# Optimization experiments

Measured on AMD Instinct MI355X. Metric: run time of the kernel, lower is better.

Reference implementation:

```python
import jax, jax.numpy as jnp
import numpy as np

FRAME_T = 8
NUM_K = 10


def _masked_att(att, temp):
    # att: [B, H, P, P] -> softmax over groups of size P//FRAME_T, top-k threshold mask
    B, H, P, _ = att.shape
    D = P // FRAME_T
    a = att.reshape(B, H, P, FRAME_T, D)
    a = jax.nn.softmax(a / temp, axis=-1)
    # k-th largest value per row as threshold (torch.topk values are sorted desc)
    margin = jax.lax.top_k(a, NUM_K)[0][..., -1]  # [B,H,P,FRAME_T]
    a = a * (a >= margin[..., None])
    return a  # [B,H,P,FRAME_T,D]


def setup_inputs() -> dict:
    key = jax.random.key(0)
    k1, k2, k3, k4 = jax.random.split(key, 4)
    B, H, P, hd = 4, 12, 1568, 64
    return {
        "att_s": jax.random.normal(k1, (B, H, P, P), dtype=jnp.float32),
        "att_t": jax.random.normal(k2, (B, H, P, P), dtype=jnp.float32),
        "v_s": jax.random.normal(k3, (B, H, P, hd), dtype=jnp.float32),
        "v_t": jax.random.normal(k4, (B, H, P, hd), dtype=jnp.float32),
    }


def reference(att_s, att_t, v_s, v_t):
    temp = jnp.float32(1.0)
    B, H, P, _ = att_t.shape
    H_s = att_s.shape[1]
    h_dim = v_t.shape[-1]
    D = P // FRAME_T

    a_s = _masked_att(att_s, temp)  # [B,Hs,P,T,D]
    a_t = _masked_att(att_t, temp)  # [B,H,P,T,D]

    vt = v_t.reshape(B, H, D, FRAME_T, h_dim)
    vs = v_s.reshape(B, H_s, D, FRAME_T, h_dim)

    norm_s = a_s.sum(-1)  # [B,Hs,P,T]
    norm_t = a_t.sum(-1)

    o_s = jnp.einsum('bhptd,bhdte->bhpte', a_s, vs) / norm_s[..., None]
    o_t = jnp.einsum('bhptd,bhdte->bhpte', a_t, vt) / norm_t[..., None]

    loss = jnp.mean((o_s - o_t) ** 2)
    return loss
```

## Files before the change

kernel.cpp:

```cpp
#include <hip/hip_runtime.h>
#include <hip/hip_bf16.h>

#define PP 1568
#define TT 8
#define DD 196
#define HD 64
#define NBH 48
#define NROW (NBH*PP*TT)
#define RPB 32
#define NBLK3 (NROW/RPB)
#define NRED1 ((NBLK3+255)/256)
#define SUB (8*DD*4)
#define VSLAB (DD*TT*HD)
#define BPB 392
#define KMASK 0xFFFFFF00u

typedef float f4 __attribute__((ext_vector_type(4)));
typedef unsigned u4 __attribute__((ext_vector_type(4)));

__device__ __forceinline__ float readlane_f(float v, int l) {
    return __int_as_float(__builtin_amdgcn_readlane(__float_as_int(v), l));
}

__device__ __forceinline__ float wave_sum_u(float v) {
#define STEPS(ctrl) { float t_ = __int_as_float(__builtin_amdgcn_update_dpp( \
        0, __float_as_int(v), ctrl, 0xF, 0xF, true)); v += t_; }
    STEPS(0x111) STEPS(0x112) STEPS(0x114) STEPS(0x118) STEPS(0x142) STEPS(0x143)
#undef STEPS
    return readlane_f(v, 63);
}

__device__ __forceinline__ unsigned UMX(unsigned a, unsigned b){ return a>b?a:b; }
__device__ __forceinline__ unsigned UMN(unsigned a, unsigned b){ return a<b?a:b; }

__device__ __forceinline__ float untr(unsigned u) {
    return (u & 0x80000000u) ? __uint_as_float(u ^ 0x80000000u)
                             : __uint_as_float(~u);
}

struct K6  { unsigned k0,k1,k2,k3,k4,k5; };
struct K10 { unsigned k0,k1,k2,k3,k4,k5,k6,k7,k8,k9; };
struct MR  { K10 f; unsigned mx; };

#define INSK(Y,C) { unsigned mx_=UMX((Y),(C)), mn_=UMN((Y),(C)); (Y)=mx_; (C)=mn_; }
#define PUTK6(Q,X,D) { unsigned b_=__float_as_uint(X); \
  unsigned u_=b_^((unsigned)((int)b_>>31)|0x80000000u); \
  unsigned c_=(u_&KMASK)|(unsigned)(D); \
  INSK(Q.k0,c_) INSK(Q.k1,c_) INSK(Q.k2,c_) INSK(Q.k3,c_) INSK(Q.k4,c_) INSK(Q.k5,c_) }
#define PUT4K6(Q,V,D0) PUTK6(Q,(V).x,(D0)) PUTK6(Q,(V).y,(D0)+1) \
                       PUTK6(Q,(V).z,(D0)+2) PUTK6(Q,(V).w,(D0)+3)

__device__ __forceinline__ K6 chain_rows(const char* stg, int a, int b8) {
    K6 q = {0,0,0,0,0,0};
    const char* rb = stg + a*784 + b8*16;
    f4 v;
    v = *(const f4*)(rb);       PUT4K6(q, v, b8*4)
    v = *(const f4*)(rb+128);   PUT4K6(q, v, b8*4+32)
    v = *(const f4*)(rb+256);   PUT4K6(q, v, b8*4+64)
    v = *(const f4*)(rb+384);   PUT4K6(q, v, b8*4+96)
    v = *(const f4*)(rb+512);   PUT4K6(q, v, b8*4+128)
    v = *(const f4*)(rb+640);   PUT4K6(q, v, b8*4+160)
    if (b8 == 7) { v = *(const f4*)(stg + a*784 + 768); PUT4K6(q, v, 192) }
    return q;
}

#define SWZ(x, pat) (unsigned)__builtin_amdgcn_ds_swizzle((int)(x), pat)
__device__ __forceinline__ K6 kshuf8_6(K6 a) {
    K6 r;
    r.k0=SWZ(a.k0,0x201F); r.k1=SWZ(a.k1,0x201F); r.k2=SWZ(a.k2,0x201F);
    r.k3=SWZ(a.k3,0x201F); r.k4=SWZ(a.k4,0x201F); r.k5=SWZ(a.k5,0x201F);
    return r;
}
__device__ __forceinline__ K10 kshuf16(K10 a) {
    K10 r;
    r.k0=SWZ(a.k0,0x401F); r.k1=SWZ(a.k1,0x401F); r.k2=SWZ(a.k2,0x401F);
    r.k3=SWZ(a.k3,0x401F); r.k4=SWZ(a.k4,0x401F); r.k5=SWZ(a.k5,0x401F);
    r.k6=SWZ(a.k6,0x401F); r.k7=SWZ(a.k7,0x401F); r.k8=SWZ(a.k8,0x401F);
    r.k9=SWZ(a.k9,0x401F);
    return r;
}
__device__ __forceinline__ K10 kbp32(K10 a, int bpx) {
    K10 r;
    r.k0=(unsigned)__builtin_amdgcn_ds_bpermute(bpx,(int)a.k0);
    r.k1=(unsigned)__builtin_amdgcn_ds_bpermute(bpx,(int)a.k1);
    r.k2=(unsigned)__builtin_amdgcn_ds_bpermute(bpx,(int)a.k2);
    r.k3=(unsigned)__builtin_amdgcn_ds_bpermute(bpx,(int)a.k3);
    r.k4=(unsigned)__builtin_amdgcn_ds_bpermute(bpx,(int)a.k4);
    r.k5=(unsigned)__builtin_amdgcn_ds_bpermute(bpx,(int)a.k5);
    r.k6=(unsigned)__builtin_amdgcn_ds_bpermute(bpx,(int)a.k6);
    r.k7=(unsigned)__builtin_amdgcn_ds_bpermute(bpx,(int)a.k7);
    r.k8=(unsigned)__builtin_amdgcn_ds_bpermute(bpx,(int)a.k8);
    r.k9=(unsigned)__builtin_amdgcn_ds_bpermute(bpx,(int)a.k9);
    return r;
}

__device__ __forceinline__ K10 kmrg66(K6 A, K6 B) {
    unsigned p00=UMN(A.k0,B.k0);
    unsigned p01=UMN(A.k0,B.k1), p10=UMN(A.k1,B.k0);
    unsigned p02=UMN(A.k0,B.k2), p11=UMN(A.k1,B.k1), p20=UMN(A.k2,B.k0);
    unsigned p03=UMN(A.k0,B.k3), p12=UMN(A.k1,B.k2), p21=UMN(A.k2,B.k1), p30=UMN(A.k3,B.k0);
    unsigned p04=UMN(A.k0,B.k4), p13=UMN(A.k1,B.k3), p22=UMN(A.k2,B.k2), p31=UMN(A.k3,B.k1), p40=UMN(A.k4,B.k0);
    unsigned p05=UMN(A.k0,B.k5), p14=UMN(A.k1,B.k4), p23=UMN(A.k2,B.k3), p32=UMN(A.k3,B.k2), p41=UMN(A.k4,B.k1), p50=UMN(A.k5,B.k0);
    unsigned p15=UMN(A.k1,B.k5), p24=UMN(A.k2,B.k4), p33=UMN(A.k3,B.k3), p42=UMN(A.k4,B.k2), p51=UMN(A.k5,B.k1);
    unsigned p25=UMN(A.k2,B.k5), p34=UMN(A.k3,B.k4), p43=UMN(A.k4,B.k3), p52=UMN(A.k5,B.k2);
    unsigned p35=UMN(A.k3,B.k5), p44=UMN(A.k4,B.k4), p53=UMN(A.k5,B.k3);
    K10 M;
    M.k0=UMX(A.k0,B.k0);
    M.k1=UMX(UMX(A.k1,B.k1),p00);
    M.k2=UMX(UMX(A.k2,B.k2),UMX(p01,p10));
    M.k3=UMX(UMX(A.k3,B.k3),UMX(p02,UMX(p11,p20)));
    M.k4=UMX(UMX(A.k4,B.k4),UMX(UMX(p03,p12),UMX(p21,p30)));
    M.k5=UMX(UMX(A.k5,B.k5),UMX(UMX(p04,p13),UMX(p22,UMX(p31,p40))));
    M.k6=UMX(UMX(p05,p14),UMX(UMX(p23,p32),UMX(p41,p50)));
    M.k7=UMX(UMX(p15,p24),UMX(p33,UMX(p42,p51)));
    M.k8=UMX(UMX(p25,p34),UMX(p43,p52));
    M.k9=UMX(p35,UMX(p44,p53));
    return M;
}

__device__ __forceinline__ K10 kmrg(K10 A, K10 B) {
    unsigned p00=UMN(A.k0,B.k0);
    unsigned p01=UMN(A.k0,B.k1), p10=UMN(A.k1,B.k0);
    unsigned p02=UMN(A.k0,B.k2), p11=UMN(A.k1,B.k1), p20=UMN(A.k2,B.k0);
    unsigned p03=UMN(A.k0,B.k3), p12=UMN(A.k1,B.k2), p21=UMN(A.k2,B.k1), p30=UMN(A.k3,B.k0);
    unsigned p04=UMN(A.k0,B.k4), p13=UMN(A.k1,B.k3), p22=UMN(A.k2,B.k2), p31=UMN(A.k3,B.k1), p40=UMN(A.k4,B.k0);
    unsigned p05=UMN(A.k0,B.k5), p14=UMN(A.k1,B.k4), p23=UMN(A.k2,B.k3), p32=UMN(A.k3,B.k2), p41=UMN(A.k4,B.k1), p50=UMN(A.k5,B.k0);
    unsigned p06=UMN(A.k0,B.k6), p15=UMN(A.k1,B.k5), p24=UMN(A.k2,B.k4), p33=UMN(A.k3,B.k3), p42=UMN(A.k4,B.k2), p51=UMN(A.k5,B.k1), p60=UMN(A.k6,B.k0);
    unsigned p07=UMN(A.k0,B.k7), p16=UMN(A.k1,B.k6), p25=UMN(A.k2,B.k5), p34=UMN(A.k3,B.k4), p43=UMN(A.k4,B.k3), p52=UMN(A.k5,B.k2), p61=UMN(A.k6,B.k1), p70=UMN(A.k7,B.k0);
    unsigned p08=UMN(A.k0,B.k8), p17=UMN(A.k1,B.k7), p26=UMN(A.k2,B.k6), p35=UMN(A.k3,B.k5), p44=UMN(A.k4,B.k4), p53=UMN(A.k5,B.k3), p62=UMN(A.k6,B.k2), p71=UMN(A.k7,B.k1), p80=UMN(A.k8,B.k0);
    K10 M;
    M.k0=UMX(A.k0,B.k0);
    M.k1=UMX(UMX(A.k1,B.k1),p00);
    M.k2=UMX(UMX(A.k2,B.k2),UMX(p01,p10));
    M.k3=UMX(UMX(A.k3,B.k3),UMX(p02,UMX(p11,p20)));
    M.k4=UMX(UMX(A.k4,B.k4),UMX(UMX(p03,p12),UMX(p21,p30)));
    M.k5=UMX(UMX(A.k5,B.k5),UMX(UMX(p04,p13),UMX(p22,UMX(p31,p40))));
    M.k6=UMX(UMX(A.k6,B.k6),UMX(UMX(p05,p14),UMX(UMX(p23,p32),UMX(p41,p50))));
    M.k7=UMX(UMX(A.k7,B.k7),UMX(UMX(UMX(p06,p15),UMX(p24,p33)),UMX(UMX(p42,p51),p60)));
    M.k8=UMX(UMX(A.k8,B.k8),UMX(UMX(UMX(p07,p16),UMX(p25,p34)),UMX(UMX(p43,p52),UMX(p61,p70))));
    M.k9=UMX(UMX(A.k9,B.k9),UMX(UMX(UMX(p08,p17),UMX(p26,p35)),UMX(UMX(p44,p53),UMX(UMX(p62,p71),p80))));
    return M;
}

__device__ __forceinline__ MR merge_all(K6 q, int bpx) {
    K10 m = kmrg66(q, kshuf8_6(q));
    K10 n = kmrg(m, kshuf16(m));
    K10 r = kbp32(n, bpx);
    MR out;
    out.mx = UMX(n.k0, r.k0);
    out.f.k0=UMX(n.k0,r.k9); out.f.k1=UMX(n.k1,r.k8); out.f.k2=UMX(n.k2,r.k7);
    out.f.k3=UMX(n.k3,r.k6); out.f.k4=UMX(n.k4,r.k5); out.f.k5=UMX(n.k5,r.k4);
    out.f.k6=UMX(n.k6,r.k3); out.f.k7=UMX(n.k7,r.k2); out.f.k8=UMX(n.k8,r.k1);
    out.f.k9=UMX(n.k9,r.k0);
    return out;
}

#define LOADR(R, P) { const char* p_=(P); \
    R##0=*(const f4*)(p_+lane*16); \
    R##1=*(const f4*)(p_+1024+lane*16); \
    R##2=*(const f4*)(p_+2048+lane*16); \
    R##3=*(const f4*)(p_+3072+lane*16); \
    R##4=*(const f4*)(p_+4096+lane*16); \
    R##5=*(const f4*)(p_+5120+lane*16); \
    if (lane<8) R##6=*(const f4*)(p_+6144+lane*16); }
#define STORER(R) { \
    *(f4*)(stg+lane*16)=R##0; *(f4*)(stg+1024+lane*16)=R##1; \
    *(f4*)(stg+2048+lane*16)=R##2; *(f4*)(stg+3072+lane*16)=R##3; \
    *(f4*)(stg+4096+lane*16)=R##4; *(f4*)(stg+5120+lane*16)=R##5; \
    if (lane<8) *(f4*)(stg+6144+lane*16)=R##6; }

#define OFS(K) ((((K)&0xFFu)<<9) + t64)

__global__ __launch_bounds__(64, 4) void vtop_main(
        const float* __restrict__ att_s, const float* __restrict__ att_t,
        const float* __restrict__ v_s,   const float* __restrict__ v_t,
        float* __restrict__ partial) {
    __shared__ f4 stgv[SUB/16];
    __shared__ f4 wbuf[5][RPB];
    __shared__ u4 obuf[5][RPB];
    char* stg = (char*)stgv;

    int lane = threadIdx.x;
    int blk  = blockIdx.x;
    int a = lane & 7, b8 = lane >> 3;
    int bpx = (lane ^ 32) << 2;

    const char* baseS = (const char*)att_s + (size_t)blk * (RPB*DD*4);
    const char* baseT = (const char*)att_t + (size_t)blk * (RPB*DD*4);

    f4 rs0{},rs1{},rs2{},rs3{},rs4{},rs5{},rs6{};
    f4 rt0{},rt1{},rt2{},rt3{},rt4{},rt5{},rt6{};

    LOADR(rs, baseS)

#pragma unroll 1
    for (int s = 0; s < 4; ++s) {
        STORER(rs)
        LOADR(rt, baseT + s*SUB)
        K6 qS = chain_rows(stg, a, b8);
        MR mS = merge_all(qS, bpx);
        STORER(rt)
        if (s < 3) LOADR(rs, baseS + (s+1)*SUB)
        K6 qT = chain_rows(stg, a, b8);
        MR mT = merge_all(qT, bpx);
        K10 fS = mS.f, fT = mT.f;

        float CS = untr(mS.mx & KMASK), CT = untr(mT.mx & KMASK);
        float wS0=__expf(untr(fS.k0&KMASK)-CS), wS1=__expf(untr(fS.k1&KMASK)-CS),
              wS2=__expf(untr(fS.k2&KMASK)-CS), wS3=__expf(untr(fS.k3&KMASK)-CS),
              wS4=__expf(untr(fS.k4&KMASK)-CS), wS5=__expf(untr(fS.k5&KMASK)-CS),
              wS6=__expf(untr(fS.k6&KMASK)-CS), wS7=__expf(untr(fS.k7&KMASK)-CS),
              wS8=__expf(untr(fS.k8&KMASK)-CS), wS9=__expf(untr(fS.k9&KMASK)-CS);
        float wT0=__expf(untr(fT.k0&KMASK)-CT), wT1=__expf(untr(fT.k1&KMASK)-CT),
              wT2=__expf(untr(fT.k2&KMASK)-CT), wT3=__expf(untr(fT.k3&KMASK)-CT),
              wT4=__expf(untr(fT.k4&KMASK)-CT), wT5=__expf(untr(fT.k5&KMASK)-CT),
              wT6=__expf(untr(fT.k6&KMASK)-CT), wT7=__expf(untr(fT.k7&KMASK)-CT),
              wT8=__expf(untr(fT.k8&KMASK)-CT), wT9=__expf(untr(fT.k9&KMASK)-CT);
        float wsS = (((wS0+wS1)+(wS2+wS3))+((wS4+wS5)+(wS6+wS7)))+(wS8+wS9);
        float wsT = (((wT0+wT1)+(wT2+wT3))+((wT4+wT5)+(wT6+wT7)))+(wT8+wT9);
        float invS =  __builtin_amdgcn_rcpf(wsS);
        float invT = -__builtin_amdgcn_rcpf(wsT);

        if (lane < 8) {
            int row = (s << 3) | lane;
            unsigned t64 = (unsigned)lane << 6;
            f4 w; u4 o;
            w.x=wS0*invS; w.y=wS1*invS; w.z=wS2*invS; w.w=wS3*invS; wbuf[0][row]=w;
            w.x=wS4*invS; w.y=wS5*invS; w.z=wS6*invS; w.w=wS7*invS; wbuf[1][row]=w;
            w.x=wS8*invS; w.y=wS9*invS; w.z=wT0*invT; w.w=wT1*invT; wbuf[2][row]=w;
            w.x=wT2*invT; w.y=wT3*invT; w.z=wT4*invT; w.w=wT5*invT; wbuf[3][row]=w;
            w.x=wT6*invT; w.y=wT7*invT; w.z=wT8*invT; w.w=wT9*invT; wbuf[4][row]=w;
            o.x=OFS(fS.k0); o.y=OFS(fS.k1); o.z=OFS(fS.k2); o.w=OFS(fS.k3); obuf[0][row]=o;
            o.x=OFS(fS.k4); o.y=OFS(fS.k5); o.z=OFS(fS.k6); o.w=OFS(fS.k7); obuf[1][row]=o;
            o.x=OFS(fS.k8); o.y=OFS(fS.k9); o.z=OFS(fT.k0); o.w=OFS(fT.k1); obuf[2][row]=o;
            o.x=OFS(fT.k2); o.y=OFS(fT.k3); o.z=OFS(fT.k4); o.w=OFS(fT.k5); obuf[3][row]=o;
            o.x=OFS(fT.k6); o.y=OFS(fT.k7); o.z=OFS(fT.k8); o.w=OFS(fT.k9); obuf[4][row]=o;
        }
    }

    int bh = blk / BPB;
    const float* vSb = v_s + (size_t)bh * VSLAB;
    const float* vTb = v_t + (size_t)bh * VSLAB;
    unsigned ul = (unsigned)lane;
    float lacc = 0.f;
#pragma unroll 1
    for (int k = 0; k < RPB; ++k) {
        f4 w0v=wbuf[0][k], w1v=wbuf[1][k], w2v=wbuf[2][k],
           w3v=wbuf[3][k], w4v=wbuf[4][k];
        u4 o0=obuf[0][k], o1=obuf[1][k], o2=obuf[2][k],
           o3=obuf[3][k], o4=obuf[4][k];
        float dsum = 0.f;
#define TERM(WC, OC, VB) dsum = fmaf(WC, VB[(size_t)((OC) + ul)], dsum);
        TERM(w0v.x, o0.x, vSb) TERM(w0v.y, o0.y, vSb)
        TERM(w0v.z, o0.z, vSb) TERM(w0v.w, o0.w, vSb)
        TERM(w1v.x, o1.x, vSb) TERM(w1v.y, o1.y, vSb)
        TERM(w1v.z, o1.z, vSb) TERM(w1v.w, o1.w, vSb)
        TERM(w2v.x, o2.x, vSb) TERM(w2v.y, o2.y, vSb)
        TERM(w2v.z, o2.z, vTb) TERM(w2v.w, o2.w, vTb)
        TERM(w3v.x, o3.x, vTb) TERM(w3v.y, o3.y, vTb)
        TERM(w3v.z, o3.z, vTb) TERM(w3v.w, o3.w, vTb)
        TERM(w4v.x, o4.x, vTb) TERM(w4v.y, o4.y, vTb)
        TERM(w4v.z, o4.z, vTb) TERM(w4v.w, o4.w, vTb)
#undef TERM
        lacc = fmaf(dsum, dsum, lacc);
    }

    float tot = wave_sum_u(lacc);
    if (lane == 0) partial[blk] = tot;
}

__global__ __launch_bounds__(256) void vtop_reduce1(
        const float* __restrict__ partial, float* __restrict__ p2) {
    int i = blockIdx.x * 256 + threadIdx.x;
    float v = (i < NBLK3) ? partial[i] : 0.f;
    float wtot = wave_sum_u(v);
    __shared__ float sm[4];
    int lane = threadIdx.x & 63, wid = threadIdx.x >> 6;
    if (lane == 0) sm[wid] = wtot;
    __syncthreads();
    if (threadIdx.x == 0) p2[blockIdx.x] = (sm[0] + sm[1]) + (sm[2] + sm[3]);
}

__global__ __launch_bounds__(256) void vtop_reduce2(
        const float* __restrict__ p2, float* __restrict__ out) {
    __shared__ double smd[256];
    double a = 0.0;
    if (threadIdx.x < NRED1) a = (double)p2[threadIdx.x];
    smd[threadIdx.x] = a;
    __syncthreads();
    for (int s = 128; s > 0; s >>= 1) {
        if (threadIdx.x < s) smd[threadIdx.x] += smd[threadIdx.x + s];
        __syncthreads();
    }
    if (threadIdx.x == 0) {
        const double inv_n = 1.0 / ((double)NBH * PP * TT * HD);
        out[0] = (float)(smd[0] * inv_n);
    }
}

extern "C" void kernel_launch(void* const* d_in, const int* in_sizes, int n_in,
                              void* d_out, int out_size, void* d_ws, size_t ws_size,
                              hipStream_t stream) {
    const float* att_s = (const float*)d_in[0];
    const float* att_t = (const float*)d_in[1];
    const float* v_s   = (const float*)d_in[2];
    const float* v_t   = (const float*)d_in[3];
    float* out     = (float*)d_out;
    float* partial = (float*)d_ws;
    float* p2      = (float*)d_ws + NBLK3;

    vtop_main<<<NBLK3, 64, 0, stream>>>(att_s, att_t, v_s, v_t, partial);
    vtop_reduce1<<<NRED1, 256, 0, stream>>>(partial, p2);
    vtop_reduce2<<<1, 256, 0, stream>>>(p2, out);
}
```

Before: 352.0 us.

## Read attention rows directly from global memory, pack four waves per block

Drops the LDS staging buffer and the register double-buffering of attention rows. Each lane now reads its strided row segments straight from global memory during the top-k chain. Blocks grow from one wave to four independent waves, each with its own weight/offset LDS slices and its own partial sum, and the reduction sizes are adjusted to match. The aim is to save the LDS round-trip and raise occupancy. In exchange the global loads become less coalesced and the explicit prefetch overlap is lost.

```diff
diff --git a/kernel.cpp b/kernel.cpp
--- a/kernel.cpp
+++ b/kernel.cpp
@@ -7,12 +7,15 @@
 #define HD 64
 #define NBH 48
 #define NROW (NBH*PP*TT)
-#define RPB 32
-#define NBLK3 (NROW/RPB)
-#define NRED1 ((NBLK3+255)/256)
+#define RPW 32
+#define WPB 4
+#define ROWS_PB (RPW*WPB)
+#define NBLK4 (NROW/ROWS_PB)
+#define NPART (NBLK4*WPB)
+#define NRED1 ((NPART+255)/256)
 #define SUB (8*DD*4)
 #define VSLAB (DD*TT*HD)
-#define BPB 392
+#define BPB 98
 #define KMASK 0xFFFFFF00u
 
 typedef float f4 __attribute__((ext_vector_type(4)));
@@ -50,9 +53,9 @@
 #define PUT4K6(Q,V,D0) PUTK6(Q,(V).x,(D0)) PUTK6(Q,(V).y,(D0)+1) \
                        PUTK6(Q,(V).z,(D0)+2) PUTK6(Q,(V).w,(D0)+3)
 
-__device__ __forceinline__ K6 chain_rows(const char* stg, int a, int b8) {
+__device__ __forceinline__ K6 chain_g(const char* base, int a, int b8) {
     K6 q = {0,0,0,0,0,0};
-    const char* rb = stg + a*784 + b8*16;
+    const char* rb = base + a*784 + b8*16;
     f4 v;
     v = *(const f4*)(rb);       PUT4K6(q, v, b8*4)
     v = *(const f4*)(rb+128);   PUT4K6(q, v, b8*4+32)
@@ -60,7 +63,7 @@
     v = *(const f4*)(rb+384);   PUT4K6(q, v, b8*4+96)
     v = *(const f4*)(rb+512);   PUT4K6(q, v, b8*4+128)
     v = *(const f4*)(rb+640);   PUT4K6(q, v, b8*4+160)
-    if (b8 == 7) { v = *(const f4*)(stg + a*784 + 768); PUT4K6(q, v, 192) }
+    if (b8 == 7) { v = *(const f4*)(base + a*784 + 768); PUT4K6(q, v, 192) }
     return q;
 }
 
@@ -155,53 +158,31 @@
     return out;
 }
 
-#define LOADR(R, P) { const char* p_=(P); \
-    R##0=*(const f4*)(p_+lane*16); \
-    R##1=*(const f4*)(p_+1024+lane*16); \
-    R##2=*(const f4*)(p_+2048+lane*16); \
-    R##3=*(const f4*)(p_+3072+lane*16); \
-    R##4=*(const f4*)(p_+4096+lane*16); \
-    R##5=*(const f4*)(p_+5120+lane*16); \
-    if (lane<8) R##6=*(const f4*)(p_+6144+lane*16); }
-#define STORER(R) { \
-    *(f4*)(stg+lane*16)=R##0; *(f4*)(stg+1024+lane*16)=R##1; \
-    *(f4*)(stg+2048+lane*16)=R##2; *(f4*)(stg+3072+lane*16)=R##3; \
-    *(f4*)(stg+4096+lane*16)=R##4; *(f4*)(stg+5120+lane*16)=R##5; \
-    if (lane<8) *(f4*)(stg+6144+lane*16)=R##6; }
-
 #define OFS(K) ((((K)&0xFFu)<<9) + t64)
 
-__global__ __launch_bounds__(64, 4) void vtop_main(
+__global__ __launch_bounds__(256, 7) void vtop_main(
         const float* __restrict__ att_s, const float* __restrict__ att_t,
         const float* __restrict__ v_s,   const float* __restrict__ v_t,
         float* __restrict__ partial) {
-    __shared__ f4 stgv[SUB/16];
-    __shared__ f4 wbuf[5][RPB];
-    __shared__ u4 obuf[5][RPB];
-    char* stg = (char*)stgv;
-
-    int lane = threadIdx.x;
-    int blk  = blockIdx.x;
+    __shared__ f4 wbuf[WPB][5][RPW];
+    __shared__ u4 obuf[WPB][5][RPW];
+
+    int tid  = threadIdx.x;
+    int wid  = tid >> 6;
+    int lane = tid & 63;
     int a = lane & 7, b8 = lane >> 3;
     int bpx = (lane ^ 32) << 2;
-
-    const char* baseS = (const char*)att_s + (size_t)blk * (RPB*DD*4);
-    const char* baseT = (const char*)att_t + (size_t)blk * (RPB*DD*4);
-
-    f4 rs0{},rs1{},rs2{},rs3{},rs4{},rs5{},rs6{};
-    f4 rt0{},rt1{},rt2{},rt3{},rt4{},rt5{},rt6{};
-
-    LOADR(rs, baseS)
+    int blk  = blockIdx.x;
+    int bh   = blk / BPB;
+
+    const char* baseS = (const char*)att_s + ((size_t)blk*ROWS_PB + wid*RPW)*(DD*4);
+    const char* baseT = (const char*)att_t + ((size_t)blk*ROWS_PB + wid*RPW)*(DD*4);
 
 #pragma unroll 1
     for (int s = 0; s < 4; ++s) {
-        STORER(rs)
-        LOADR(rt, baseT + s*SUB)
-        K6 qS = chain_rows(stg, a, b8);
+        K6 qS = chain_g(baseS + s*SUB, a, b8);
         MR mS = merge_all(qS, bpx);
-        STORER(rt)
-        if (s < 3) LOADR(rs, baseS + (s+1)*SUB)
-        K6 qT = chain_rows(stg, a, b8);
+        K6 qT = chain_g(baseT + s*SUB, a, b8);
         MR mT = merge_all(qT, bpx);
         K10 fS = mS.f, fT = mT.f;
 
@@ -225,30 +206,29 @@
             int row = (s << 3) | lane;
             unsigned t64 = (unsigned)lane << 6;
             f4 w; u4 o;
-            w.x=wS0*invS; w.y=wS1*invS; w.z=wS2*invS; w.w=wS3*invS; wbuf[0][row]=w;
-            w.x=wS4*invS; w.y=wS5*invS; w.z=wS6*invS; w.w=wS7*invS; wbuf[1][row]=w;
-            w.x=wS8*invS; w.y=wS9*invS; w.z=wT0*invT; w.w=wT1*invT; wbuf[2][row]=w;
-            w.x=wT2*invT; w.y=wT3*invT; w.z=wT4*invT; w.w=wT5*invT; wbuf[3][row]=w;
-            w.x=wT6*invT; w.y=wT7*invT; w.z=wT8*invT; w.w=wT9*invT; wbuf[4][row]=w;
-            o.x=OFS(fS.k0); o.y=OFS(fS.k1); o.z=OFS(fS.k2); o.w=OFS(fS.k3); obuf[0][row]=o;
-            o.x=OFS(fS.k4); o.y=OFS(fS.k5); o.z=OFS(fS.k6); o.w=OFS(fS.k7); obuf[1][row]=o;
-            o.x=OFS(fS.k8); o.y=OFS(fS.k9); o.z=OFS(fT.k0); o.w=OFS(fT.k1); obuf[2][row]=o;
-            o.x=OFS(fT.k2); o.y=OFS(fT.k3); o.z=OFS(fT.k4); o.w=OFS(fT.k5); obuf[3][row]=o;
-            o.x=OFS(fT.k6); o.y=OFS(fT.k7); o.z=OFS(fT.k8); o.w=OFS(fT.k9); obuf[4][row]=o;
+            w.x=wS0*invS; w.y=wS1*invS; w.z=wS2*invS; w.w=wS3*invS; wbuf[wid][0][row]=w;
+            w.x=wS4*invS; w.y=wS5*invS; w.z=wS6*invS; w.w=wS7*invS; wbuf[wid][1][row]=w;
+            w.x=wS8*invS; w.y=wS9*invS; w.z=wT0*invT; w.w=wT1*invT; wbuf[wid][2][row]=w;
+            w.x=wT2*invT; w.y=wT3*invT; w.z=wT4*invT; w.w=wT5*invT; wbuf[wid][3][row]=w;
+            w.x=wT6*invT; w.y=wT7*invT; w.z=wT8*invT; w.w=wT9*invT; wbuf[wid][4][row]=w;
+            o.x=OFS(fS.k0); o.y=OFS(fS.k1); o.z=OFS(fS.k2); o.w=OFS(fS.k3); obuf[wid][0][row]=o;
+            o.x=OFS(fS.k4); o.y=OFS(fS.k5); o.z=OFS(fS.k6); o.w=OFS(fS.k7); obuf[wid][1][row]=o;
+            o.x=OFS(fS.k8); o.y=OFS(fS.k9); o.z=OFS(fT.k0); o.w=OFS(fT.k1); obuf[wid][2][row]=o;
+            o.x=OFS(fT.k2); o.y=OFS(fT.k3); o.z=OFS(fT.k4); o.w=OFS(fT.k5); obuf[wid][3][row]=o;
+            o.x=OFS(fT.k6); o.y=OFS(fT.k7); o.z=OFS(fT.k8); o.w=OFS(fT.k9); obuf[wid][4][row]=o;
         }
     }
 
-    int bh = blk / BPB;
     const float* vSb = v_s + (size_t)bh * VSLAB;
     const float* vTb = v_t + (size_t)bh * VSLAB;
     unsigned ul = (unsigned)lane;
     float lacc = 0.f;
 #pragma unroll 1
-    for (int k = 0; k < RPB; ++k) {
-        f4 w0v=wbuf[0][k], w1v=wbuf[1][k], w2v=wbuf[2][k],
-           w3v=wbuf[3][k], w4v=wbuf[4][k];
-        u4 o0=obuf[0][k], o1=obuf[1][k], o2=obuf[2][k],
-           o3=obuf[3][k], o4=obuf[4][k];
+    for (int k = 0; k < RPW; ++k) {
+        f4 w0v=wbuf[wid][0][k], w1v=wbuf[wid][1][k], w2v=wbuf[wid][2][k],
+           w3v=wbuf[wid][3][k], w4v=wbuf[wid][4][k];
+        u4 o0=obuf[wid][0][k], o1=obuf[wid][1][k], o2=obuf[wid][2][k],
+           o3=obuf[wid][3][k], o4=obuf[wid][4][k];
         float dsum = 0.f;
 #define TERM(WC, OC, VB) dsum = fmaf(WC, VB[(size_t)((OC) + ul)], dsum);
         TERM(w0v.x, o0.x, vSb) TERM(w0v.y, o0.y, vSb)
@@ -266,13 +246,13 @@
     }
 
     float tot = wave_sum_u(lacc);
-    if (lane == 0) partial[blk] = tot;
+    if (lane == 0) partial[blk * WPB + wid] = tot;
 }
 
 __global__ __launch_bounds__(256) void vtop_reduce1(
         const float* __restrict__ partial, float* __restrict__ p2) {
     int i = blockIdx.x * 256 + threadIdx.x;
-    float v = (i < NBLK3) ? partial[i] : 0.f;
+    float v = (i < NPART) ? partial[i] : 0.f;
     float wtot = wave_sum_u(v);
     __shared__ float sm[4];
     int lane = threadIdx.x & 63, wid = threadIdx.x >> 6;
@@ -307,9 +287,9 @@
     const float* v_t   = (const float*)d_in[3];
     float* out     = (float*)d_out;
     float* partial = (float*)d_ws;
-    float* p2      = (float*)d_ws + NBLK3;
-
-    vtop_main<<<NBLK3, 64, 0, stream>>>(att_s, att_t, v_s, v_t, partial);
+    float* p2      = (float*)d_ws + NPART;
+
+    vtop_main<<<NBLK4, 256, 0, stream>>>(att_s, att_t, v_s, v_t, partial);
     vtop_reduce1<<<NRED1, 256, 0, stream>>>(partial, p2);
     vtop_reduce2<<<1, 256, 0, stream>>>(p2, out);
 }
```

New measurement: 590.1 us. +67.6%, slower.
